# Performance work log

Hardware: AMD Instinct MI355X
Metric: run time of the kernel (lower is better)

The kernel has to match this reference:

```python
import jax, jax.numpy as jnp
import numpy as np
from jax.ops import segment_sum
import math

N = 100_000
E = 1_600_000
D = 128          # node_feature_dim
HID = 128        # hidden_dim
H = 4            # num_heads
HD = HID // H    # head_dim


def setup_inputs() -> dict:
    key = jax.random.key(0)
    ks = jax.random.split(key, 12)
    s = 0.02
    return {
        "node_features": jax.random.normal(ks[0], (N, D), dtype=jnp.float32),
        "edge_index": jax.random.randint(ks[1], (2, E), 0, N, dtype=jnp.int32),
        "edge_weights": jax.random.uniform(ks[2], (E,), dtype=jnp.float32),
        "Wq": jax.random.normal(ks[3], (D, HID), dtype=jnp.float32) * s,
        "bq": jnp.zeros((HID,), dtype=jnp.float32),
        "Wk": jax.random.normal(ks[4], (D, HID), dtype=jnp.float32) * s,
        "bk": jnp.zeros((HID,), dtype=jnp.float32),
        "Wv": jax.random.normal(ks[5], (D, HID), dtype=jnp.float32) * s,
        "bv": jnp.zeros((HID,), dtype=jnp.float32),
        "Wo": jax.random.normal(ks[6], (HID, HID), dtype=jnp.float32) * s,
        "bo": jnp.zeros((HID,), dtype=jnp.float32),
        "We": jax.random.normal(ks[7], (H,), dtype=jnp.float32) * s,  # edge_proj weight, Linear(1, H)
        "be": jnp.zeros((H,), dtype=jnp.float32),
    }


def reference(node_features, edge_index, edge_weights,
              Wq, bq, Wk, bk, Wv, bv, Wo, bo, We, be):
    scale = math.sqrt(HD)
    Q = (node_features @ Wq + bq).reshape(N, H, HD)
    K = (node_features @ Wk + bk).reshape(N, H, HD)
    V = (node_features @ Wv + bv).reshape(N, H, HD)

    src, tgt = edge_index[0], edge_index[1]

    # per-edge attention scores (E, H)
    scores = jnp.einsum("ehd,ehd->eh", Q[tgt], K[src]) / scale
    # edge_proj: Linear(1, H) applied to edge_weights[:, None]
    scores = scores + edge_weights[:, None] * We[None, :] + be[None, :]

    # scatter softmax over target nodes
    max_scores = jnp.full((N, H), -1e9, dtype=scores.dtype).at[tgt].max(scores)
    exp_scores = jnp.exp(scores - max_scores[tgt])
    sum_exp = segment_sum(exp_scores, tgt, num_segments=N)
    probs = exp_scores / (sum_exp[tgt] + 1e-8)

    # weighted scatter-sum aggregation
    out = jnp.zeros((N, H, HD), dtype=scores.dtype).at[tgt].add(probs[:, :, None] * V[src])
    return out.reshape(N, HID) @ Wo + bo
```

## Files before the change

### kernel.cpp

```cpp
#include <hip/hip_runtime.h>

#define N_NODES 100000
#define E_EDGES 1600000

typedef unsigned short u16;
typedef unsigned int   u32;
typedef unsigned char  u8;
typedef float f32x4  __attribute__((ext_vector_type(4)));
typedef short bf16x8 __attribute__((ext_vector_type(8)));

#define NBUK 98
#define BCAP 20480

__device__ __forceinline__ u16 f2b(float f) {
  u32 b = __float_as_uint(f);
  return (u16)((b + 0x7FFFu + ((b >> 16) & 1u)) >> 16);
}
__device__ __forceinline__ float blo(u32 u) { return __uint_as_float(u << 16); }
__device__ __forceinline__ float bhi(u32 u) { return __uint_as_float(u & 0xFFFF0000u); }

__device__ __forceinline__ u8 f2e4m3(float f) {
  u32 b = __float_as_uint(f);
  u32 s = (b >> 24) & 0x80u;
  float y = __uint_as_float(b & 0x7fffffffu) * 0x1p-120f;
  u32 u = __float_as_uint(y);
  u += 0x7FFFFu + ((u >> 20) & 1u);
  return (u8)(s | ((u >> 20) & 0x7fu));
}

__device__ __forceinline__ float e4m3_1(u32 x) {
  u32 y = ((x & 0x80u) << 24) | ((x & 0x7fu) << 20);
  return __uint_as_float(y) * 0x1p120f;
}

__device__ __forceinline__ void dec4(u32 kq, float& k0, float& k1, float& k2, float& k3) {
#if __has_builtin(__builtin_amdgcn_cvt_pk_f32_fp8)
  auto lo = __builtin_amdgcn_cvt_pk_f32_fp8((int)kq, false);
  auto hi = __builtin_amdgcn_cvt_pk_f32_fp8((int)kq, true);
  k0 = lo[0]; k1 = lo[1]; k2 = hi[0]; k3 = hi[1];
#else
  k0 = e4m3_1(kq); k1 = e4m3_1(kq >> 8); k2 = e4m3_1(kq >> 16); k3 = e4m3_1(kq >> 24);
#endif
}

template<int CTRL>
__device__ __forceinline__ float dpp_add(float d) {
  int x = __builtin_amdgcn_update_dpp(0, __float_as_int(d), CTRL, 0xf, 0xf, true);
  return d + __int_as_float(x);
}
__device__ __forceinline__ float reduce8(float d) {
  d = dpp_add<0xB1>(d);
  d = dpp_add<0x4E>(d);
  d = dpp_add<0x141>(d);
  return d;
}

__global__ __launch_bounds__(256) void setup(
    const float* __restrict__ Wq, const float* __restrict__ Wk,
    const float* __restrict__ Wv, const float* __restrict__ Wo,
    u16* __restrict__ Wt, u32* __restrict__ bcur)
{
  int tid = blockIdx.x * 256 + threadIdx.x;
  if (tid < NBUK) bcur[tid] = (u32)tid * BCAP;
  int idx = tid - NBUK;
  if (idx >= 0 && idx < 65536) {
    int mat = idx >> 14;
    int rem = idx & 16383;
    int n = rem >> 7, k = rem & 127;
    const float* W = (mat == 0) ? Wq : (mat == 1) ? Wk : (mat == 2) ? Wv : Wo;
    Wt[idx] = f2b(W[k * 128 + n]);
  }
}

__global__ __launch_bounds__(256) void gemm_qkv(
    const float* __restrict__ A, const u16* __restrict__ Wt,
    const float* __restrict__ bq, const float* __restrict__ bk,
    const float* __restrict__ bv,
    u16* __restrict__ Qb, u8* __restrict__ Kf8, u16* __restrict__ Vb16, int M)
{
  __shared__ u16 Alds[64][136];
  __shared__ u16 Blds[128][136];
  const int t = threadIdx.x;
  const int row0 = blockIdx.x * 64;

#pragma unroll
  for (int i = 0; i < 8; ++i) {
    int f = t + i * 256;
    int r = f >> 5, c4 = f & 31;
    int gr = row0 + r; if (gr >= M) gr = M - 1;
    float4 v = ((const float4*)(A + (size_t)gr * 128))[c4];
    u32* dst = (u32*)&Alds[r][c4 * 4];
    dst[0] = (u32)f2b(v.x) | ((u32)f2b(v.y) << 16);
    dst[1] = (u32)f2b(v.z) | ((u32)f2b(v.w) << 16);
  }

  const int lane = t & 63;
  const int mrow = lane & 15;
  const int q    = lane >> 4;
  const int m0   = (t >> 6) * 16;

  for (int m = 0; m < 3; ++m) {
    __syncthreads();
#pragma unroll
    for (int i = 0; i < 8; ++i) {
      int f = t + i * 256;
      int r = f >> 4, c8 = f & 15;
      uint4 v = ((const uint4*)(Wt + (size_t)m * 16384 + (size_t)r * 128))[c8];
      *(uint4*)&Blds[r][c8 * 8] = v;
    }
    __syncthreads();

    f32x4 acc[8];
#pragma unroll
    for (int c = 0; c < 8; ++c) acc[c] = (f32x4){0.f, 0.f, 0.f, 0.f};
#pragma unroll
    for (int kk = 0; kk < 4; ++kk) {
      const int kb = kk * 32 + q * 8;
      bf16x8 a = *(const bf16x8*)&Alds[m0 + mrow][kb];
#pragma unroll
      for (int c = 0; c < 8; ++c) {
        bf16x8 b = *(const bf16x8*)&Blds[c * 16 + mrow][kb];
        acc[c] = __builtin_amdgcn_mfma_f32_16x16x32_bf16(a, b, acc[c], 0, 0, 0);
      }
    }

    const float* bias = (m == 0) ? bq : (m == 1) ? bk : bv;
#pragma unroll
    for (int c = 0; c < 8; ++c) {
      int gcol = c * 16 + mrow;
      float bvv = bias[gcol];
#pragma unroll
      for (int r = 0; r < 4; ++r) {
        int grow = row0 + m0 + q * 4 + r;
        if (grow < M) {
          float outv = acc[c][r] + bvv;
          if (m == 0) {
            Qb[(size_t)grow * 128 + gcol] = f2b(outv);
          } else if (m == 1) {
            Kf8[(size_t)grow * 128 + gcol] = f2e4m3(outv);
          } else {
            Vb16[(size_t)grow * 128 + gcol] = f2b(outv);
          }
        }
      }
    }
  }
}

__global__ __launch_bounds__(256) void gemm_out(
    const u16* __restrict__ A, const u16* __restrict__ Wt,
    const float* __restrict__ bias, float* __restrict__ Cout, int M)
{
  __shared__ u16 Alds[64][136];
  __shared__ u16 Blds[128][136];
  const int t = threadIdx.x;
  const int row0 = blockIdx.x * 64;

#pragma unroll
  for (int i = 0; i < 4; ++i) {
    int f = t + i * 256;
    int r = f >> 4, c8 = f & 15;
    int gr = row0 + r; if (gr >= M) gr = M - 1;
    uint4 v = ((const uint4*)(A + (size_t)gr * 128))[c8];
    *(uint4*)&Alds[r][c8 * 8] = v;
  }
#pragma unroll
  for (int i = 0; i < 8; ++i) {
    int f = t + i * 256;
    int r = f >> 4, c8 = f & 15;
    uint4 v = ((const uint4*)(Wt + (size_t)r * 128))[c8];
    *(uint4*)&Blds[r][c8 * 8] = v;
  }
  __syncthreads();

  const int lane = t & 63;
  const int mrow = lane & 15;
  const int q    = lane >> 4;
  const int m0   = (t >> 6) * 16;

  f32x4 acc[8];
#pragma unroll
  for (int c = 0; c < 8; ++c) acc[c] = (f32x4){0.f, 0.f, 0.f, 0.f};
#pragma unroll
  for (int kk = 0; kk < 4; ++kk) {
    const int kb = kk * 32 + q * 8;
    bf16x8 a = *(const bf16x8*)&Alds[m0 + mrow][kb];
#pragma unroll
    for (int c = 0; c < 8; ++c) {
      bf16x8 b = *(const bf16x8*)&Blds[c * 16 + mrow][kb];
      acc[c] = __builtin_amdgcn_mfma_f32_16x16x32_bf16(a, b, acc[c], 0, 0, 0);
    }
  }

#pragma unroll
  for (int c = 0; c < 8; ++c) {
    int gcol = c * 16 + mrow;
    float bv = bias[gcol];
#pragma unroll
    for (int r = 0; r < 4; ++r) {
      int grow = row0 + m0 + q * 4 + r;
      if (grow < M) Cout[(size_t)grow * 128 + gcol] = acc[c][r] + bv;
    }
  }
}

__global__ __launch_bounds__(256) void pass1_bin(
    const int* __restrict__ ei, const float* __restrict__ ew,
    u32* __restrict__ bcur, uint2* __restrict__ stag)
{
  __shared__ u32 s_px[4096];
  __shared__ u32 s_py[4096];
  __shared__ u32 s_gp[4096];
  __shared__ u32 s_hist[NBUK];
  __shared__ u32 s_excl[NBUK];
  __shared__ u32 s_gbase[NBUK];
  __shared__ u32 s_wsum[4];
  const int t = threadIdx.x;
  const int base = blockIdx.x * 4096;
  const int nv = min(4096, E_EDGES - base);

  if (t < NBUK) s_hist[t] = 0;
  __syncthreads();

  u32 tg[16], py[16];
  const int4*   src4 = (const int4*)(ei + base);
  const int4*   tgt4 = (const int4*)(ei + E_EDGES + base);
  const float4* ewv4 = (const float4*)(ew + base);
#pragma unroll
  for (int j = 0; j < 4; ++j) {
    int q4 = t + j * 256;
    bool valid = (q4 * 4) < nv;
    int qq = valid ? q4 : 0;
    int4   sv = src4[qq];
    int4   tv = tgt4[qq];
    float4 wv = ewv4[qq];
    u32* TG = &tg[j * 4];
    u32* PY = &py[j * 4];
    TG[0] = (u32)tv.x; TG[1] = (u32)tv.y; TG[2] = (u32)tv.z; TG[3] = (u32)tv.w;
    PY[0] = ((u32)sv.x << 15) | (u32)(wv.x * 32768.0f);
    PY[1] = ((u32)sv.y << 15) | (u32)(wv.y * 32768.0f);
    PY[2] = ((u32)sv.z << 15) | (u32)(wv.z * 32768.0f);
    PY[3] = ((u32)sv.w << 15) | (u32)(wv.w * 32768.0f);
    if (valid) {
      atomicAdd(&s_hist[TG[0] >> 10], 1u);
      atomicAdd(&s_hist[TG[1] >> 10], 1u);
      atomicAdd(&s_hist[TG[2] >> 10], 1u);
      atomicAdd(&s_hist[TG[3] >> 10], 1u);
    } else {
      TG[0] = TG[1] = TG[2] = TG[3] = 0xFFFFFFFFu;
    }
  }
  __syncthreads();

  {
    int v = (t < NBUK) ? (int)s_hist[t] : 0;
    int x = v;
#pragma unroll
    for (int d = 1; d < 64; d <<= 1) {
      int y = __shfl_up(x, d, 64);
      if ((t & 63) >= d) x += y;
    }
    if ((t & 63) == 63 && t < 128) s_wsum[t >> 6] = (u32)x;
    __syncthreads();
    if (t < NBUK) {
      int incl = x + ((t >= 64) ? (int)s_wsum[0] : 0);
      s_excl[t] = (u32)(incl - v);
      s_gbase[t] = (v > 0) ? atomicAdd(&bcur[t], (u32)v) : 0u;
    }
  }
  __syncthreads();
  if (t < NBUK) s_hist[t] = s_excl[t];
  __syncthreads();

#pragma unroll
  for (int i = 0; i < 16; ++i) {
    if (tg[i] != 0xFFFFFFFFu) {
      u32 bk = tg[i] >> 10;
      u32 lp = atomicAdd(&s_hist[bk], 1u);
      s_px[lp] = tg[i];
      s_py[lp] = py[i];
      s_gp[lp] = s_gbase[bk] + (lp - s_excl[bk]);
    }
  }
  __syncthreads();
  for (int s = t; s < nv; s += 256)
    stag[s_gp[s]] = make_uint2(s_px[s], s_py[s]);
}

__global__ __launch_bounds__(1024) void pass2_scatter(
    const u32* __restrict__ bcur, const uint2* __restrict__ stag,
    int2* __restrict__ nodeinfo, u32* __restrict__ csr)
{
  __shared__ int s_hist[1024];
  __shared__ int s_wsum[16];
  const int t = threadIdx.x;
  const int b = blockIdx.x;
  const int sb = b * BCAP;
  const int cnt = (int)bcur[b] - sb;
  const int node_base = b << 10;

  s_hist[t] = 0;
  __syncthreads();

  int i = t;
  for (; i + 3072 < cnt; i += 4096) {
    uint2 e0 = stag[sb + i];
    uint2 e1 = stag[sb + i + 1024];
    uint2 e2 = stag[sb + i + 2048];
    uint2 e3 = stag[sb + i + 3072];
    atomicAdd(&s_hist[e0.x & 1023], 1);
    atomicAdd(&s_hist[e1.x & 1023], 1);
    atomicAdd(&s_hist[e2.x & 1023], 1);
    atomicAdd(&s_hist[e3.x & 1023], 1);
  }
  for (; i < cnt; i += 1024)
    atomicAdd(&s_hist[stag[sb + i].x & 1023], 1);
  __syncthreads();

  int v = s_hist[t];
  int x = v;
#pragma unroll
  for (int d = 1; d < 64; d <<= 1) {
    int y = __shfl_up(x, d, 64);
    if ((t & 63) >= d) x += y;
  }
  if ((t & 63) == 63) s_wsum[t >> 6] = x;
  __syncthreads();
  if (t < 64) {
    int w = (t < 16) ? s_wsum[t] : 0;
#pragma unroll
    for (int d = 1; d < 16; d <<= 1) {
      int y = __shfl_up(w, d, 64);
      if (t >= d) w += y;
    }
    if (t < 16) s_wsum[t] = w;
  }
  __syncthreads();
  int wbase = (t >= 64) ? s_wsum[(t >> 6) - 1] : 0;
  int excl = x + wbase - v;
  int node = node_base + t;
  if (node < N_NODES) nodeinfo[node] = make_int2(sb + excl, v);
  __syncthreads();
  s_hist[t] = sb + excl;
  __syncthreads();

  i = t;
  for (; i + 3072 < cnt; i += 4096) {
    uint2 e0 = stag[sb + i];
    uint2 e1 = stag[sb + i + 1024];
    uint2 e2 = stag[sb + i + 2048];
    uint2 e3 = stag[sb + i + 3072];
    int p0 = atomicAdd(&s_hist[e0.x & 1023], 1);
    int p1 = atomicAdd(&s_hist[e1.x & 1023], 1);
    int p2 = atomicAdd(&s_hist[e2.x & 1023], 1);
    int p3 = atomicAdd(&s_hist[e3.x & 1023], 1);
    csr[p0] = e0.y;
    csr[p1] = e1.y;
    csr[p2] = e2.y;
    csr[p3] = e3.y;
  }
  for (; i < cnt; i += 1024) {
    uint2 pr = stag[sb + i];
    int pos = atomicAdd(&s_hist[pr.x & 1023], 1);
    csr[pos] = pr.y;
  }
}

__global__ __launch_bounds__(256) void gather_fused(
    const int2* __restrict__ nodeinfo, const u32* __restrict__ csr,
    u32* __restrict__ Qb32, const u8* __restrict__ Kf8,
    const u32* __restrict__ Vb,
    const float* __restrict__ We, const float* __restrict__ be)
{
  int node = blockIdx.x * 4 + (threadIdx.x >> 6);
  int l    = threadIdx.x & 63;
  int half = l >> 5;
  int hl   = l & 31;
  int h    = hl >> 3;

  const float scale = 0.17677669529663687f;
  const float eiq   = 1.0f / 32768.0f;
  uint2 qp = *(const uint2*)(Qb32 + (size_t)node * 64 + hl * 2);
  float qa = blo(qp.x) * scale, qb = bhi(qp.x) * scale;
  float qc = blo(qp.y) * scale, qd = bhi(qp.y) * scale;
  float weq = We[h] * eiq, bE = be[h];
  const u32 laneK = (u32)hl * 4;
  const u32 laneV = (u32)hl * 8;

  int2 ni = nodeinfo[node];
  int s0 = ni.x, L = ni.y;
  int npair = L >> 1;
  const u32* cp = csr + s0 + half;
  const char* Kc = (const char*)Kf8;
  const char* Vc = (const char*)Vb;

  float a0 = 0.f, a1 = 0.f, a2 = 0.f, a3 = 0.f, sum = 0.f;

  auto LDK = [&](u32 c) -> u32 {
    return *(const u32*)(Kc + (((c >> 15) << 7) + laneK));
  };
  auto LDV = [&](u32 c) -> uint2 {
    return *(const uint2*)(Vc + (((c >> 15) << 8) + laneV));
  };
  auto COMP = [&](u32 c, u32 kq, uint2 vv) {
    float k0, k1, k2, k3;
    dec4(kq, k0, k1, k2, k3);
    float d = qa * k0 + qb * k1 + qc * k2 + qd * k3;
    d = reduce8(d);
    float p = __expf(d + (float)(c & 32767u) * weq + bE);
    sum += p;
    a0 += p * blo(vv.x);
    a1 += p * bhi(vv.x);
    a2 += p * blo(vv.y);
    a3 += p * bhi(vv.y);
  };

  int i = 0;
  for (; i + 4 <= npair; i += 4) {
    u32 c0 = cp[2 * i];
    u32 c1 = cp[2 * i + 2];
    u32 c2 = cp[2 * i + 4];
    u32 c3 = cp[2 * i + 6];
    u32 k0 = LDK(c0), k1 = LDK(c1), k2 = LDK(c2), k3 = LDK(c3);
    uint2 v0 = LDV(c0), v1 = LDV(c1), v2 = LDV(c2), v3 = LDV(c3);
    COMP(c0, k0, v0);
    COMP(c1, k1, v1);
    COMP(c2, k2, v2);
    COMP(c3, k3, v3);
  }
  for (; i < npair; ++i) {
    u32 c = cp[2 * i];
    u32 kq = LDK(c);
    uint2 vv = LDV(c);
    COMP(c, kq, vv);
  }
  if (L & 1) {
    u32 c = csr[s0 + L - 1];
    u32 kq = LDK(c);
    uint2 vv = LDV(c);
    float k0, k1, k2, k3;
    dec4(kq, k0, k1, k2, k3);
    float d = qa * k0 + qb * k1 + qc * k2 + qd * k3;
    d = reduce8(d);
    float p = __expf(d + (float)(c & 32767u) * weq + bE);
    p = half ? 0.f : p;
    sum += p;
    a0 += p * blo(vv.x);
    a1 += p * bhi(vv.x);
    a2 += p * blo(vv.y);
    a3 += p * bhi(vv.y);
  }

  sum += __shfl_xor(sum, 32, 64);
  a0  += __shfl_xor(a0, 32, 64);
  a1  += __shfl_xor(a1, 32, 64);
  a2  += __shfl_xor(a2, 32, 64);
  a3  += __shfl_xor(a3, 32, 64);

  float inv = 1.f / (sum + 1e-8f);
  if (half == 0) {
    uint2 w;
    w.x = (u32)f2b(a0 * inv) | ((u32)f2b(a1 * inv) << 16);
    w.y = (u32)f2b(a2 * inv) | ((u32)f2b(a3 * inv) << 16);
    *(uint2*)(Qb32 + (size_t)node * 64 + hl * 2) = w;
  }
}

extern "C" void kernel_launch(void* const* d_in, const int* in_sizes, int n_in,
                              void* d_out, int out_size, void* d_ws, size_t ws_size,
                              hipStream_t stream) {
  const float* nf = (const float*)d_in[0];
  const int*   ei = (const int*)  d_in[1];
  const float* ew = (const float*)d_in[2];
  const float* Wq = (const float*)d_in[3];
  const float* bq = (const float*)d_in[4];
  const float* Wk = (const float*)d_in[5];
  const float* bk = (const float*)d_in[6];
  const float* Wv = (const float*)d_in[7];
  const float* bv = (const float*)d_in[8];
  const float* Wo = (const float*)d_in[9];
  const float* bo = (const float*)d_in[10];
  const float* We = (const float*)d_in[11];
  const float* be = (const float*)d_in[12];
  float* out = (float*)d_out;

  char* ws = (char*)d_ws;
  u16*  Wt  = (u16*)ws;
  u16*  Qb  = (u16*)(ws + 131072);
  u8*   Kf8 = (u8*)(Qb + (size_t)N_NODES * 128);
  u16*  Vb16 = (u16*)(Kf8 + (size_t)N_NODES * 128);
  char* p   = (char*)(Vb16 + (size_t)N_NODES * 128);
  uint2* stag = (uint2*)p;              p += (size_t)NBUK * BCAP * 8;
  u32*  csr = (u32*)p;                  p += (size_t)NBUK * BCAP * 4;
  int2* nodeinfo = (int2*)p;            p += (size_t)N_NODES * 8;
  u32*  bcur = (u32*)p;                 p += 512;

  const int echunks = (E_EDGES + 4095) / 4096;

  setup<<<(NBUK + 65536 + 255) / 256, 256, 0, stream>>>(Wq, Wk, Wv, Wo, Wt, bcur);

  const int mblocks = (N_NODES + 63) / 64;
  gemm_qkv<<<mblocks, 256, 0, stream>>>(nf, Wt, bq, bk, bv, Qb, Kf8, Vb16, N_NODES);

  pass1_bin<<<echunks, 256, 0, stream>>>(ei, ew, bcur, stag);
  pass2_scatter<<<NBUK, 1024, 0, stream>>>(bcur, stag, nodeinfo, csr);

  gather_fused<<<N_NODES / 4, 256, 0, stream>>>(nodeinfo, csr,
      (u32*)Qb, Kf8, (const u32*)Vb16, We, be);

  gemm_out<<<mblocks, 256, 0, stream>>>(Qb, Wt + 49152, bo, out, N_NODES);
}
```

Measured before the change: 321.6 us.

## Merge QKV GEMM with edge binning and stage GEMM outputs through LDS

The QKV projection GEMM and the first edge-binning pass now run as one launch, with block ranges split between the two roles, so the independent pieces of work overlap and one kernel launch is dropped. Both GEMM epilogues now stage results in shared memory and write whole rows with 16-byte stores, replacing scattered 1- and 2-byte global writes. pass2_scatter keeps its staged edges in registers (up to 20 per thread) and reads them from global memory once instead of twice. In exchange, register pressure rises, the fused kernel uses about 52KB of shared memory per block, and a bucket with more than 20480 edges would not be fully handled.

```diff
diff --git a/kernel.cpp b/kernel.cpp
--- a/kernel.cpp
+++ b/kernel.cpp
@@ -11,6 +11,8 @@
 
 #define NBUK 98
 #define BCAP 20480
+#define MBLOCKS 1563
+#define ECHUNKS 391
 
 __device__ __forceinline__ u16 f2b(float f) {
   u32 b = __float_as_uint(f);
@@ -72,78 +74,187 @@
   }
 }
 
-__global__ __launch_bounds__(256) void gemm_qkv(
+__global__ __launch_bounds__(256) void qkv_pass1(
     const float* __restrict__ A, const u16* __restrict__ Wt,
     const float* __restrict__ bq, const float* __restrict__ bk,
     const float* __restrict__ bv,
-    u16* __restrict__ Qb, u8* __restrict__ Kf8, u16* __restrict__ Vb16, int M)
+    u16* __restrict__ Qb, u8* __restrict__ Kf8, u16* __restrict__ Vb16, int M,
+    const int* __restrict__ ei, const float* __restrict__ ew,
+    u32* __restrict__ bcur, uint2* __restrict__ stag)
 {
-  __shared__ u16 Alds[64][136];
-  __shared__ u16 Blds[128][136];
+  __shared__ __align__(16) char smem[52224];
   const int t = threadIdx.x;
-  const int row0 = blockIdx.x * 64;
-
-#pragma unroll
-  for (int i = 0; i < 8; ++i) {
-    int f = t + i * 256;
-    int r = f >> 5, c4 = f & 31;
-    int gr = row0 + r; if (gr >= M) gr = M - 1;
-    float4 v = ((const float4*)(A + (size_t)gr * 128))[c4];
-    u32* dst = (u32*)&Alds[r][c4 * 4];
-    dst[0] = (u32)f2b(v.x) | ((u32)f2b(v.y) << 16);
-    dst[1] = (u32)f2b(v.z) | ((u32)f2b(v.w) << 16);
-  }
-
-  const int lane = t & 63;
-  const int mrow = lane & 15;
-  const int q    = lane >> 4;
-  const int m0   = (t >> 6) * 16;
-
-  for (int m = 0; m < 3; ++m) {
-    __syncthreads();
+
+  if ((int)blockIdx.x < MBLOCKS) {
+    typedef u16 row136[136];
+    row136* Alds = (row136*)smem;
+    row136* Blds = (row136*)(smem + 17408);
+    const int row0 = blockIdx.x * 64;
+
 #pragma unroll
     for (int i = 0; i < 8; ++i) {
       int f = t + i * 256;
-      int r = f >> 4, c8 = f & 15;
-      uint4 v = ((const uint4*)(Wt + (size_t)m * 16384 + (size_t)r * 128))[c8];
-      *(uint4*)&Blds[r][c8 * 8] = v;
-    }
+      int r = f >> 5, c4 = f & 31;
+      int gr = row0 + r; if (gr >= M) gr = M - 1;
+      float4 v = ((const float4*)(A + (size_t)gr * 128))[c4];
+      u32* dst = (u32*)&Alds[r][c4 * 4];
+      dst[0] = (u32)f2b(v.x) | ((u32)f2b(v.y) << 16);
+      dst[1] = (u32)f2b(v.z) | ((u32)f2b(v.w) << 16);
+    }
+
+    const int lane = t & 63;
+    const int mrow = lane & 15;
+    const int q    = lane >> 4;
+    const int m0   = (t >> 6) * 16;
+
+    for (int m = 0; m < 3; ++m) {
+      __syncthreads();
+#pragma unroll
+      for (int i = 0; i < 8; ++i) {
+        int f = t + i * 256;
+        int r = f >> 4, c8 = f & 15;
+        uint4 v = ((const uint4*)(Wt + (size_t)m * 16384 + (size_t)r * 128))[c8];
+        *(uint4*)&Blds[r][c8 * 8] = v;
+      }
+      __syncthreads();
+
+      f32x4 acc[8];
+#pragma unroll
+      for (int c = 0; c < 8; ++c) acc[c] = (f32x4){0.f, 0.f, 0.f, 0.f};
+#pragma unroll
+      for (int kk = 0; kk < 4; ++kk) {
+        const int kb = kk * 32 + q * 8;
+        bf16x8 a = *(const bf16x8*)&Alds[m0 + mrow][kb];
+#pragma unroll
+        for (int c = 0; c < 8; ++c) {
+          bf16x8 b = *(const bf16x8*)&Blds[c * 16 + mrow][kb];
+          acc[c] = __builtin_amdgcn_mfma_f32_16x16x32_bf16(a, b, acc[c], 0, 0, 0);
+        }
+      }
+
+      const float* bias = (m == 0) ? bq : (m == 1) ? bk : bv;
+      __syncthreads();
+      if (m == 1) {
+        u8* Kst = (u8*)Blds;
+#pragma unroll
+        for (int c = 0; c < 8; ++c) {
+          int gcol = c * 16 + mrow;
+          float bvv = bias[gcol];
+#pragma unroll
+          for (int r = 0; r < 4; ++r)
+            Kst[(m0 + q * 4 + r) * 128 + gcol] = f2e4m3(acc[c][r] + bvv);
+        }
+        __syncthreads();
+#pragma unroll
+        for (int i = 0; i < 2; ++i) {
+          int f = t + i * 256;
+          int r = f >> 3, c16 = f & 7;
+          int grow = row0 + r;
+          if (grow < M)
+            *(uint4*)(Kf8 + (size_t)grow * 128 + c16 * 16) =
+                *(const uint4*)(Kst + r * 128 + c16 * 16);
+        }
+      } else {
+        u16* St = (u16*)Blds;
+#pragma unroll
+        for (int c = 0; c < 8; ++c) {
+          int gcol = c * 16 + mrow;
+          float bvv = bias[gcol];
+#pragma unroll
+          for (int r = 0; r < 4; ++r)
+            St[(m0 + q * 4 + r) * 128 + gcol] = f2b(acc[c][r] + bvv);
+        }
+        __syncthreads();
+        u16* dstM = (m == 0) ? Qb : Vb16;
+#pragma unroll
+        for (int i = 0; i < 4; ++i) {
+          int f = t + i * 256;
+          int r = f >> 4, c8 = f & 15;
+          int grow = row0 + r;
+          if (grow < M)
+            *(uint4*)(dstM + (size_t)grow * 128 + c8 * 8) =
+                *(const uint4*)(St + r * 128 + c8 * 8);
+        }
+      }
+    }
+  } else {
+    u32* s_px    = (u32*)smem;
+    u32* s_py    = (u32*)(smem + 16384);
+    u32* s_gp    = (u32*)(smem + 32768);
+    u32* s_hist  = (u32*)(smem + 49152);
+    u32* s_excl  = (u32*)(smem + 49544);
+    u32* s_gbase = (u32*)(smem + 49936);
+    u32* s_wsum  = (u32*)(smem + 50328);
+
+    const int base = ((int)blockIdx.x - MBLOCKS) * 4096;
+    const int nv = min(4096, E_EDGES - base);
+
+    if (t < NBUK) s_hist[t] = 0;
     __syncthreads();
 
-    f32x4 acc[8];
-#pragma unroll
-    for (int c = 0; c < 8; ++c) acc[c] = (f32x4){0.f, 0.f, 0.f, 0.f};
-#pragma unroll
-    for (int kk = 0; kk < 4; ++kk) {
-      const int kb = kk * 32 + q * 8;
-      bf16x8 a = *(const bf16x8*)&Alds[m0 + mrow][kb];
-#pragma unroll
-      for (int c = 0; c < 8; ++c) {
-        bf16x8 b = *(const bf16x8*)&Blds[c * 16 + mrow][kb];
-        acc[c] = __builtin_amdgcn_mfma_f32_16x16x32_bf16(a, b, acc[c], 0, 0, 0);
-      }
-    }
-
-    const float* bias = (m == 0) ? bq : (m == 1) ? bk : bv;
-#pragma unroll
-    for (int c = 0; c < 8; ++c) {
-      int gcol = c * 16 + mrow;
-      float bvv = bias[gcol];
-#pragma unroll
-      for (int r = 0; r < 4; ++r) {
-        int grow = row0 + m0 + q * 4 + r;
-        if (grow < M) {
-          float outv = acc[c][r] + bvv;
-          if (m == 0) {
-            Qb[(size_t)grow * 128 + gcol] = f2b(outv);
-          } else if (m == 1) {
-            Kf8[(size_t)grow * 128 + gcol] = f2e4m3(outv);
-          } else {
-            Vb16[(size_t)grow * 128 + gcol] = f2b(outv);
-          }
-        }
-      }
-    }
+    u32 tg[16], py[16];
+    const int4*   src4 = (const int4*)(ei + base);
+    const int4*   tgt4 = (const int4*)(ei + E_EDGES + base);
+    const float4* ewv4 = (const float4*)(ew + base);
+#pragma unroll
+    for (int j = 0; j < 4; ++j) {
+      int q4 = t + j * 256;
+      bool valid = (q4 * 4) < nv;
+      int qq = valid ? q4 : 0;
+      int4   sv = src4[qq];
+      int4   tv = tgt4[qq];
+      float4 wv = ewv4[qq];
+      u32* TG = &tg[j * 4];
+      u32* PY = &py[j * 4];
+      TG[0] = (u32)tv.x; TG[1] = (u32)tv.y; TG[2] = (u32)tv.z; TG[3] = (u32)tv.w;
+      PY[0] = ((u32)sv.x << 15) | (u32)(wv.x * 32768.0f);
+      PY[1] = ((u32)sv.y << 15) | (u32)(wv.y * 32768.0f);
+      PY[2] = ((u32)sv.z << 15) | (u32)(wv.z * 32768.0f);
+      PY[3] = ((u32)sv.w << 15) | (u32)(wv.w * 32768.0f);
+      if (valid) {
+        atomicAdd(&s_hist[TG[0] >> 10], 1u);
+        atomicAdd(&s_hist[TG[1] >> 10], 1u);
+        atomicAdd(&s_hist[TG[2] >> 10], 1u);
+        atomicAdd(&s_hist[TG[3] >> 10], 1u);
+      } else {
+        TG[0] = TG[1] = TG[2] = TG[3] = 0xFFFFFFFFu;
+      }
+    }
+    __syncthreads();
+
+    {
+      int v = (t < NBUK) ? (int)s_hist[t] : 0;
+      int x = v;
+#pragma unroll
+      for (int d = 1; d < 64; d <<= 1) {
+        int y = __shfl_up(x, d, 64);
+        if ((t & 63) >= d) x += y;
+      }
+      if ((t & 63) == 63 && t < 128) s_wsum[t >> 6] = (u32)x;
+      __syncthreads();
+      if (t < NBUK) {
+        int incl = x + ((t >= 64) ? (int)s_wsum[0] : 0);
+        s_excl[t] = (u32)(incl - v);
+        s_gbase[t] = (v > 0) ? atomicAdd(&bcur[t], (u32)v) : 0u;
+      }
+    }
+    __syncthreads();
+    if (t < NBUK) s_hist[t] = s_excl[t];
+    __syncthreads();
+
+#pragma unroll
+    for (int i = 0; i < 16; ++i) {
+      if (tg[i] != 0xFFFFFFFFu) {
+        u32 bk = tg[i] >> 10;
+        u32 lp = atomicAdd(&s_hist[bk], 1u);
+        s_px[lp] = tg[i];
+        s_py[lp] = py[i];
+        s_gp[lp] = s_gbase[bk] + (lp - s_excl[bk]);
+      }
+    }
+    __syncthreads();
+    for (int s = t; s < nv; s += 256)
+      stag[s_gp[s]] = make_uint2(s_px[s], s_py[s]);
   }
 }
 
@@ -151,8 +262,8 @@
     const u16* __restrict__ A, const u16* __restrict__ Wt,
     const float* __restrict__ bias, float* __restrict__ Cout, int M)
 {
-  __shared__ u16 Alds[64][136];
-  __shared__ u16 Blds[128][136];
+  __shared__ __align__(16) u16 Alds[64][136];
+  __shared__ __align__(16) u16 Blds[128][136];
   const int t = threadIdx.x;
   const int row0 = blockIdx.x * 64;
 
@@ -192,99 +303,26 @@
     }
   }
 
+  __syncthreads();
+  float* Fst = (float*)&Blds[0][0];
 #pragma unroll
   for (int c = 0; c < 8; ++c) {
     int gcol = c * 16 + mrow;
     float bv = bias[gcol];
 #pragma unroll
-    for (int r = 0; r < 4; ++r) {
-      int grow = row0 + m0 + q * 4 + r;
-      if (grow < M) Cout[(size_t)grow * 128 + gcol] = acc[c][r] + bv;
-    }
-  }
-}
-
-__global__ __launch_bounds__(256) void pass1_bin(
-    const int* __restrict__ ei, const float* __restrict__ ew,
-    u32* __restrict__ bcur, uint2* __restrict__ stag)
-{
-  __shared__ u32 s_px[4096];
-  __shared__ u32 s_py[4096];
-  __shared__ u32 s_gp[4096];
-  __shared__ u32 s_hist[NBUK];
-  __shared__ u32 s_excl[NBUK];
-  __shared__ u32 s_gbase[NBUK];
-  __shared__ u32 s_wsum[4];
-  const int t = threadIdx.x;
-  const int base = blockIdx.x * 4096;
-  const int nv = min(4096, E_EDGES - base);
-
-  if (t < NBUK) s_hist[t] = 0;
-  __syncthreads();
-
-  u32 tg[16], py[16];
-  const int4*   src4 = (const int4*)(ei + base);
-  const int4*   tgt4 = (const int4*)(ei + E_EDGES + base);
-  const float4* ewv4 = (const float4*)(ew + base);
-#pragma unroll
-  for (int j = 0; j < 4; ++j) {
-    int q4 = t + j * 256;
-    bool valid = (q4 * 4) < nv;
-    int qq = valid ? q4 : 0;
-    int4   sv = src4[qq];
-    int4   tv = tgt4[qq];
-    float4 wv = ewv4[qq];
-    u32* TG = &tg[j * 4];
-    u32* PY = &py[j * 4];
-    TG[0] = (u32)tv.x; TG[1] = (u32)tv.y; TG[2] = (u32)tv.z; TG[3] = (u32)tv.w;
-    PY[0] = ((u32)sv.x << 15) | (u32)(wv.x * 32768.0f);
-    PY[1] = ((u32)sv.y << 15) | (u32)(wv.y * 32768.0f);
-    PY[2] = ((u32)sv.z << 15) | (u32)(wv.z * 32768.0f);
-    PY[3] = ((u32)sv.w << 15) | (u32)(wv.w * 32768.0f);
-    if (valid) {
-      atomicAdd(&s_hist[TG[0] >> 10], 1u);
-      atomicAdd(&s_hist[TG[1] >> 10], 1u);
-      atomicAdd(&s_hist[TG[2] >> 10], 1u);
-      atomicAdd(&s_hist[TG[3] >> 10], 1u);
-    } else {
-      TG[0] = TG[1] = TG[2] = TG[3] = 0xFFFFFFFFu;
-    }
-  }
-  __syncthreads();
-
-  {
-    int v = (t < NBUK) ? (int)s_hist[t] : 0;
-    int x = v;
-#pragma unroll
-    for (int d = 1; d < 64; d <<= 1) {
-      int y = __shfl_up(x, d, 64);
-      if ((t & 63) >= d) x += y;
-    }
-    if ((t & 63) == 63 && t < 128) s_wsum[t >> 6] = (u32)x;
-    __syncthreads();
-    if (t < NBUK) {
-      int incl = x + ((t >= 64) ? (int)s_wsum[0] : 0);
-      s_excl[t] = (u32)(incl - v);
-      s_gbase[t] = (v > 0) ? atomicAdd(&bcur[t], (u32)v) : 0u;
-    }
-  }
-  __syncthreads();
-  if (t < NBUK) s_hist[t] = s_excl[t];
-  __syncthreads();
-
-#pragma unroll
-  for (int i = 0; i < 16; ++i) {
-    if (tg[i] != 0xFFFFFFFFu) {
-      u32 bk = tg[i] >> 10;
-      u32 lp = atomicAdd(&s_hist[bk], 1u);
-      s_px[lp] = tg[i];
-      s_py[lp] = py[i];
-      s_gp[lp] = s_gbase[bk] + (lp - s_excl[bk]);
-    }
-  }
-  __syncthreads();
-  for (int s = t; s < nv; s += 256)
-    stag[s_gp[s]] = make_uint2(s_px[s], s_py[s]);
+    for (int r = 0; r < 4; ++r)
+      Fst[(m0 + q * 4 + r) * 132 + gcol] = acc[c][r] + bv;
+  }
+  __syncthreads();
+#pragma unroll
+  for (int i = 0; i < 8; ++i) {
+    int f = t + i * 256;
+    int r = f >> 5, c4 = f & 31;
+    int grow = row0 + r;
+    if (grow < M)
+      *(float4*)(Cout + (size_t)grow * 128 + c4 * 4) =
+          *(const float4*)(Fst + r * 132 + c4 * 4);
+  }
 }
 
 __global__ __launch_bounds__(1024) void pass2_scatter(
@@ -302,19 +340,20 @@
   s_hist[t] = 0;
   __syncthreads();
 
-  int i = t;
-  for (; i + 3072 < cnt; i += 4096) {
-    uint2 e0 = stag[sb + i];
-    uint2 e1 = stag[sb + i + 1024];
-    uint2 e2 = stag[sb + i + 2048];
-    uint2 e3 = stag[sb + i + 3072];
-    atomicAdd(&s_hist[e0.x & 1023], 1);
-    atomicAdd(&s_hist[e1.x & 1023], 1);
-    atomicAdd(&s_hist[e2.x & 1023], 1);
-    atomicAdd(&s_hist[e3.x & 1023], 1);
-  }
-  for (; i < cnt; i += 1024)
-    atomicAdd(&s_hist[stag[sb + i].x & 1023], 1);
+  u32 tgr[20], pyr[20];
+#pragma unroll
+  for (int k = 0; k < 20; ++k) {
+    int i = t + k * 1024;
+    if (i < cnt) {
+      uint2 e = stag[sb + i];
+      tgr[k] = e.x & 1023u;
+      pyr[k] = e.y;
+      atomicAdd(&s_hist[tgr[k]], 1);
+    } else {
+      tgr[k] = 0xFFFFFFFFu;
+      pyr[k] = 0u;
+    }
+  }
   __syncthreads();
 
   int v = s_hist[t];
@@ -344,25 +383,12 @@
   s_hist[t] = sb + excl;
   __syncthreads();
 
-  i = t;
-  for (; i + 3072 < cnt; i += 4096) {
-    uint2 e0 = stag[sb + i];
-    uint2 e1 = stag[sb + i + 1024];
-    uint2 e2 = stag[sb + i + 2048];
-    uint2 e3 = stag[sb + i + 3072];
-    int p0 = atomicAdd(&s_hist[e0.x & 1023], 1);
-    int p1 = atomicAdd(&s_hist[e1.x & 1023], 1);
-    int p2 = atomicAdd(&s_hist[e2.x & 1023], 1);
-    int p3 = atomicAdd(&s_hist[e3.x & 1023], 1);
-    csr[p0] = e0.y;
-    csr[p1] = e1.y;
-    csr[p2] = e2.y;
-    csr[p3] = e3.y;
-  }
-  for (; i < cnt; i += 1024) {
-    uint2 pr = stag[sb + i];
-    int pos = atomicAdd(&s_hist[pr.x & 1023], 1);
-    csr[pos] = pr.y;
+#pragma unroll
+  for (int k = 0; k < 20; ++k) {
+    if (tgr[k] != 0xFFFFFFFFu) {
+      int pos = atomicAdd(&s_hist[tgr[k]], 1);
+      csr[pos] = pyr[k];
+    }
   }
 }
 
@@ -495,18 +521,15 @@
   int2* nodeinfo = (int2*)p;            p += (size_t)N_NODES * 8;
   u32*  bcur = (u32*)p;                 p += 512;
 
-  const int echunks = (E_EDGES + 4095) / 4096;
-
   setup<<<(NBUK + 65536 + 255) / 256, 256, 0, stream>>>(Wq, Wk, Wv, Wo, Wt, bcur);
 
-  const int mblocks = (N_NODES + 63) / 64;
-  gemm_qkv<<<mblocks, 256, 0, stream>>>(nf, Wt, bq, bk, bv, Qb, Kf8, Vb16, N_NODES);
-
-  pass1_bin<<<echunks, 256, 0, stream>>>(ei, ew, bcur, stag);
+  qkv_pass1<<<MBLOCKS + ECHUNKS, 256, 0, stream>>>(
+      nf, Wt, bq, bk, bv, Qb, Kf8, Vb16, N_NODES, ei, ew, bcur, stag);
+
   pass2_scatter<<<NBUK, 1024, 0, stream>>>(bcur, stag, nodeinfo, csr);
 
   gather_fused<<<N_NODES / 4, 256, 0, stream>>>(nodeinfo, csr,
       (u32*)Qb, Kf8, (const u32*)Vb16, We, be);
 
-  gemm_out<<<mblocks, 256, 0, stream>>>(Qb, Wt + 49152, bo, out, N_NODES);
-}
+  gemm_out<<<MBLOCKS, 256, 0, stream>>>(Qb, Wt + 49152, bo, out, N_NODES);
+}
```

Result: faster. 275.3 us (-14.4%).
